# Kernel optimization log

Hardware: AMD Instinct MI355X
Metric: run time of the kernel (lower is better)

The kernel has to match this reference:

```python
import jax, jax.numpy as jnp
import numpy as np

N_USERS_P1 = 50001
N_ITEMS_P1 = 100001
N = N_USERS_P1 + N_ITEMS_P1  # 150002
D = 64
N_BEH = 2
N_LAYERS = 2
N_EDGES = 2000000
BATCH = 2048
REG_WEIGHT = 1e-4
EPS = 1e-9
GAMMA = 1e-10  # BPRLoss gamma


def setup_inputs() -> dict:
    key = jax.random.key(0)
    ks = jax.random.split(key, 12)
    return {
        "user_emb": jax.random.normal(ks[0], (N_USERS_P1, D), jnp.float32) * 0.1,
        "item_emb": jax.random.normal(ks[1], (N_ITEMS_P1, D), jnp.float32) * 0.1,
        "now_degree": jax.random.uniform(ks[2], (N_BEH, N, 1), jnp.float32, 1.0, 100.0),
        "old_degree": jax.random.uniform(ks[3], (N_BEH, N, 1), jnp.float32, 1.0, 100.0),
        "last_stage": jax.random.normal(ks[4], (N_BEH, N_LAYERS, N, D), jnp.float32) * 0.1,
        "denom_w": jax.random.uniform(ks[5], (1,), jnp.float32),
        "oldscale_w": jax.random.uniform(ks[6], (1,), jnp.float32),
        "conv_w": jax.random.normal(ks[7], (N_BEH, N_LAYERS, 2), jnp.float32),
        "src": jax.random.randint(ks[8], (N_BEH, N_EDGES), 0, N, jnp.int32),
        "dst": jax.random.randint(ks[9], (N_BEH, N_EDGES), 0, N, jnp.int32),
        "batch_data": jax.random.randint(ks[10], (BATCH, N_BEH, 3), 1, N_USERS_P1, jnp.int32),
    }


def _propagate(user_emb, item_emb, now_degree, old_degree, last_stage,
               denom_w, oldscale_w, conv_w, src, dst):
    total = jnp.concatenate([user_emb, item_emb], axis=0)  # [N, D]
    n = total.shape[0]
    all_embeddings = []
    for b in range(N_BEH):
        # denominator_forward: ReLU(W*old) + new ; molecular = ones
        den = jnp.sqrt(jax.nn.relu(old_degree[b] * denom_w[0]) + now_degree[b])  # [N,1]
        norm = 1.0 / (den + EPS)  # [N,1] (molecular == 1)
        e = total
        layer_embs = [e]
        for _ in range(N_LAYERS):
            e = norm * e
            # sparse adjacency matmul: scatter-add gathered rows (binary adjacency)
            e = jax.ops.segment_sum(e[src[b]], dst[b], num_segments=n)
            e = norm * e
            layer_embs.append(e)
        # oldscale_forward + rescale of last-stage embeddings
        old_scale = jnp.sqrt(jax.nn.relu(old_degree[b] * oldscale_w[0]))  # [N,1]
        rscale = old_scale / (den + EPS)  # [N,1]
        new_layers = [total]
        for l in range(N_LAYERS):
            old_l = last_stage[b, l] * rscale
            # Conv2d(1,1,(2,1)) over stacked (old,new): w0*old + w1*new
            new_layers.append(conv_w[b, l, 0] * old_l + conv_w[b, l, 1] * layer_embs[l])
        mean_e = jnp.stack(new_layers, axis=1).mean(axis=1)  # [N, D]
        # F.normalize(dim=-1)
        mean_e = mean_e / jnp.maximum(jnp.linalg.norm(mean_e, axis=-1, keepdims=True), 1e-12)
        total = mean_e + total
        all_embeddings.append(total)
    return all_embeddings


def reference(user_emb, item_emb, now_degree, old_degree, last_stage,
              denom_w, oldscale_w, conv_w, src, dst, batch_data):
    all_embeddings = _propagate(user_emb, item_emb, now_degree, old_degree,
                                last_stage, denom_w, oldscale_w, conv_w, src, dst)
    total_loss = jnp.float32(0.0)
    for b in range(N_BEH):
        emb = all_embeddings[b]
        u_all = emb[:N_USERS_P1]
        i_all = emb[N_USERS_P1:]
        data = batch_data[:, b]
        uf = u_all[data[:, 0]]          # [B, D]
        itf = i_all[data[:, 1:]]        # [B, 2, D]
        scores = jnp.einsum('bd,bkd->bk', uf, itf)  # [B, 2]
        bpr = -jnp.log(GAMMA + jax.nn.sigmoid(scores[:, 0] - scores[:, 1])).mean()
        total_loss = total_loss + bpr
    # EmbLoss: sum of L2 norms / last embedding's row count
    emb_loss = (jnp.linalg.norm(user_emb) + jnp.linalg.norm(item_emb)) / item_emb.shape[0]
    return total_loss + REG_WEIGHT * emb_loss
```

## Files before the change

### kernel.cpp

```cpp
#include <hip/hip_runtime.h>

#define N_USERS_P1 50001
#define N_ITEMS_P1 100001
#define N_TOTAL    150002
#define DIM        64
#define N_BEH      2
#define N_EDGES    2000000
#define BATCH      2048
#define ND         ((long)N_TOTAL * DIM)
#define REG_WEIGHT 1e-4f
#define GAMMA_     1e-10f
#define EPS_       1e-9f

#define SCAN_CHUNK 1024
#define NB_SCAN    ((N_TOTAL + SCAN_CHUNK - 1) / SCAN_CHUNK)

#define FILL_G     256
#define FILL_NB    (8 * FILL_G)

__global__ void I_CRGCN_57002805952693_kernel() {}

__global__ void k_init(float* __restrict__ accums, float* __restrict__ out) {
    if (threadIdx.x < 4) accums[threadIdx.x] = 0.f;
    if (threadIdx.x == 0) out[0] = 0.25f;
}

__global__ void k_zero4(float4* __restrict__ p, long n4) {
    long i = (long)blockIdx.x * blockDim.x + threadIdx.x;
    long s = (long)gridDim.x * blockDim.x;
    float4 z = make_float4(0.f, 0.f, 0.f, 0.f);
    for (; i < n4; i += s) p[i] = z;
}

__global__ void k_zero_int(int* __restrict__ p, int n) {
    int i = blockIdx.x * blockDim.x + threadIdx.x;
    if (i < n) p[i] = 0;
}

__global__ void k_build_total(const float* __restrict__ ue,
                              const float* __restrict__ ie,
                              float* __restrict__ total,
                              float* __restrict__ accums) {
    const long NU = (long)N_USERS_P1 * DIM;
    long i = (long)blockIdx.x * blockDim.x + threadIdx.x;
    long s = (long)gridDim.x * blockDim.x;
    float su = 0.f, si = 0.f;
    for (; i < ND; i += s) {
        float v;
        if (i < NU) { v = ue[i];      su += v * v; }
        else        { v = ie[i - NU]; si += v * v; }
        total[i] = v;
    }
    for (int o = 32; o > 0; o >>= 1) {
        su += __shfl_xor(su, o);
        si += __shfl_xor(si, o);
    }
    __shared__ float smu[4], smi[4];
    int w = threadIdx.x >> 6, l = threadIdx.x & 63;
    if (l == 0) { smu[w] = su; smi[w] = si; }
    __syncthreads();
    if (threadIdx.x == 0) {
        float a = 0.f, b = 0.f;
        for (int k = 0; k < 4; k++) { a += smu[k]; b += smi[k]; }
        atomicAdd(&accums[0], a);
        atomicAdd(&accums[1], b);
    }
}

__global__ void k_norms(const float* __restrict__ now_deg,
                        const float* __restrict__ old_deg,
                        const float* __restrict__ denom_w,
                        const float* __restrict__ oldscale_w,
                        float* __restrict__ norm,
                        float* __restrict__ rscale) {
    int i = blockIdx.x * blockDim.x + threadIdx.x;
    if (i >= N_BEH * N_TOTAL) return;
    float dw = denom_w[0], ow = oldscale_w[0];
    float od = old_deg[i], nd = now_deg[i];
    float den = sqrtf(fmaxf(od * dw, 0.f) + nd);
    float inv = 1.f / (den + EPS_);
    norm[i]   = inv;
    rscale[i] = sqrtf(fmaxf(od * ow, 0.f)) * inv;
}

__global__ void k_count(const int* __restrict__ dst, int* __restrict__ deg) {
    int i = blockIdx.x * blockDim.x + threadIdx.x;
    if (i < N_EDGES) atomicAdd(&deg[dst[i]], 1);
}

__global__ void k_count_pos(const int* __restrict__ dst,
                            int* __restrict__ deg,
                            unsigned char* __restrict__ pos) {
    int i = blockIdx.x * blockDim.x + threadIdx.x;
    if (i < N_EDGES) {
        int p = atomicAdd(&deg[dst[i]], 1);
        pos[i] = (unsigned char)p;
    }
}

__global__ void k_scan1(const int* __restrict__ deg,
                        int* __restrict__ rowptr,
                        int* __restrict__ bsum) {
    __shared__ int sh[256];
    int tid  = threadIdx.x;
    int base = blockIdx.x * SCAN_CHUNK + tid * 4;
    int v0 = 0, v1 = 0, v2 = 0, v3 = 0;
    if (base + 0 < N_TOTAL) v0 = deg[base + 0];
    if (base + 1 < N_TOTAL) v1 = deg[base + 1];
    if (base + 2 < N_TOTAL) v2 = deg[base + 2];
    if (base + 3 < N_TOTAL) v3 = deg[base + 3];
    int s = v0 + v1 + v2 + v3;
    sh[tid] = s;
    __syncthreads();
    for (int off = 1; off < 256; off <<= 1) {
        int t = (tid >= off) ? sh[tid - off] : 0;
        __syncthreads();
        sh[tid] += t;
        __syncthreads();
    }
    int excl = sh[tid] - s;
    if (base + 0 < N_TOTAL) rowptr[base + 0] = excl;
    if (base + 1 < N_TOTAL) rowptr[base + 1] = excl + v0;
    if (base + 2 < N_TOTAL) rowptr[base + 2] = excl + v0 + v1;
    if (base + 3 < N_TOTAL) rowptr[base + 3] = excl + v0 + v1 + v2;
    if (tid == 255) bsum[blockIdx.x] = sh[255];
}

__global__ void k_scan1_ip(int* __restrict__ data, int* __restrict__ bsum) {
    __shared__ int sh[256];
    int tid  = threadIdx.x;
    int base = blockIdx.x * SCAN_CHUNK + tid * 4;
    int v0 = 0, v1 = 0, v2 = 0, v3 = 0;
    if (base + 0 < N_TOTAL) v0 = data[base + 0];
    if (base + 1 < N_TOTAL) v1 = data[base + 1];
    if (base + 2 < N_TOTAL) v2 = data[base + 2];
    if (base + 3 < N_TOTAL) v3 = data[base + 3];
    int s = v0 + v1 + v2 + v3;
    sh[tid] = s;
    __syncthreads();
    for (int off = 1; off < 256; off <<= 1) {
        int t = (tid >= off) ? sh[tid - off] : 0;
        __syncthreads();
        sh[tid] += t;
        __syncthreads();
    }
    int excl = sh[tid] - s;
    if (base + 0 < N_TOTAL) data[base + 0] = excl;
    if (base + 1 < N_TOTAL) data[base + 1] = excl + v0;
    if (base + 2 < N_TOTAL) data[base + 2] = excl + v0 + v1;
    if (base + 3 < N_TOTAL) data[base + 3] = excl + v0 + v1 + v2;
    if (tid == 255) bsum[blockIdx.x] = sh[255];
}

__global__ void k_scan2(int* __restrict__ bsum) {
    __shared__ int sh[256];
    int tid = threadIdx.x;
    int v = (tid < NB_SCAN) ? bsum[tid] : 0;
    sh[tid] = v;
    __syncthreads();
    for (int off = 1; off < 256; off <<= 1) {
        int t = (tid >= off) ? sh[tid - off] : 0;
        __syncthreads();
        sh[tid] += t;
        __syncthreads();
    }
    if (tid < NB_SCAN) bsum[tid] = sh[tid] - v;
}

__global__ void k_scan3(int* __restrict__ rowptr, const int* __restrict__ bsum,
                        int* __restrict__ cursor) {
    int i = blockIdx.x * blockDim.x + threadIdx.x;
    if (i >= N_TOTAL) return;
    int v = rowptr[i] + bsum[i / SCAN_CHUNK];
    rowptr[i] = v;
    cursor[i] = v;
}

__global__ void k_scan3a(int* __restrict__ rowptr, const int* __restrict__ bsum) {
    int i = blockIdx.x * blockDim.x + threadIdx.x;
    if (i == 0) rowptr[N_TOTAL] = N_EDGES;
    if (i >= N_TOTAL) return;
    rowptr[i] += bsum[i / SCAN_CHUNK];
}

__global__ void k_fill(const int* __restrict__ src, const int* __restrict__ dst,
                       int* __restrict__ cursor, int* __restrict__ csr_src) {
    int i = blockIdx.x * blockDim.x + threadIdx.x;
    if (i < N_EDGES) {
        int pos = atomicAdd(&cursor[dst[i]], 1);
        csr_src[pos] = src[i];
    }
}

__global__ void k_fill_banded(const int* __restrict__ src,
                              const int* __restrict__ dst,
                              const int* __restrict__ rowptr,
                              const unsigned char* __restrict__ pos,
                              int* __restrict__ csr) {
    const int C = (N_EDGES + FILL_G - 1) / FILL_G;
    int x = blockIdx.x & 7;
    int g = blockIdx.x >> 3;
    int beg = g * C;
    int end = beg + C;
    if (end > N_EDGES) end = N_EDGES;
    for (int i = beg + threadIdx.x; i < end; i += blockDim.x) {
        int d = dst[i];
        if (((d >> 12) & 7) == x) {
            csr[rowptr[d] + (int)pos[i]] = src[i];
        }
    }
}

__global__ void k_gather_update(const int* __restrict__ rowptr,
                                const int* __restrict__ rowend,
                                const int* __restrict__ csr_src,
                                const float* __restrict__ norm,
                                const float* __restrict__ rscale,
                                const float* __restrict__ tin,
                                float* __restrict__ tout,
                                const float* __restrict__ last_b,
                                const float* __restrict__ conv_b) {
    long gid  = (long)blockIdx.x * blockDim.x + threadIdx.x;
    long row  = gid >> 6;
    int  lane = (int)(gid & 63);
    if (row >= N_TOTAL) return;
    int beg = rowptr[row], end = rowend[row];
    float acc = 0.f;
    int j = beg;
    for (; j + 4 <= end; j += 4) {
        int s0 = csr_src[j], s1 = csr_src[j + 1];
        int s2 = csr_src[j + 2], s3 = csr_src[j + 3];
        float a0 = norm[s0] * tin[(long)s0 * DIM + lane];
        float a1 = norm[s1] * tin[(long)s1 * DIM + lane];
        float a2 = norm[s2] * tin[(long)s2 * DIM + lane];
        float a3 = norm[s3] * tin[(long)s3 * DIM + lane];
        acc += a0 + a1 + a2 + a3;
    }
    for (; j < end; ++j) {
        int s = csr_src[j];
        acc += norm[s] * tin[(long)s * DIM + lane];
    }
    float cw00 = conv_b[0], cw01 = conv_b[1];
    float cw10 = conv_b[2], cw11 = conv_b[3];
    long  off = row * DIM + lane;
    float t   = tin[off];
    float e1  = norm[row] * acc;
    float ls0 = last_b[off];
    float ls1 = last_b[ND + off];
    float rs  = rscale[row];
    float m = (t + cw00 * ls0 * rs + cw01 * t + cw10 * ls1 * rs + cw11 * e1)
              * (1.f / 3.f);
    float ss = m * m;
    for (int o = 32; o > 0; o >>= 1) ss += __shfl_xor(ss, o);
    tout[off] = t + m / fmaxf(sqrtf(ss), 1e-12f);
}

__global__ void k_edges(const int* __restrict__ src,
                        const int* __restrict__ dst,
                        const float* __restrict__ norm,
                        const float* __restrict__ total,
                        float* __restrict__ agg) {
    long gid   = (long)blockIdx.x * blockDim.x + threadIdx.x;
    long wave  = gid >> 6;
    int  lane  = (int)(gid & 63);
    long waves = ((long)gridDim.x * blockDim.x) >> 6;
    for (long e = wave; e < N_EDGES; e += waves) {
        int s = src[e], t = dst[e];
        float v = norm[s] * total[(long)s * DIM + lane];
        atomicAdd(&agg[(long)t * DIM + lane], v);
    }
}

__global__ void k_update(float* __restrict__ total,
                         const float* __restrict__ agg,
                         const float* __restrict__ norm,
                         const float* __restrict__ rscale,
                         const float* __restrict__ last_b,
                         const float* __restrict__ conv_b) {
    long gid  = (long)blockIdx.x * blockDim.x + threadIdx.x;
    long row  = gid >> 6;
    int  lane = (int)(gid & 63);
    if (row >= N_TOTAL) return;
    float cw00 = conv_b[0], cw01 = conv_b[1];
    float cw10 = conv_b[2], cw11 = conv_b[3];
    long  off = row * DIM + lane;
    float t   = total[off];
    float e1  = norm[row] * agg[off];
    float ls0 = last_b[off];
    float ls1 = last_b[ND + off];
    float rs  = rscale[row];
    float m = (t + cw00 * ls0 * rs + cw01 * t + cw10 * ls1 * rs + cw11 * e1)
              * (1.f / 3.f);
    float ss = m * m;
    for (int o = 32; o > 0; o >>= 1) ss += __shfl_xor(ss, o);
    total[off] = t + m / fmaxf(sqrtf(ss), 1e-12f);
}

__global__ void k_bpr(const float* __restrict__ total,
                      const int* __restrict__ bdata,
                      int b,
                      float* __restrict__ acc) {
    long gid  = (long)blockIdx.x * blockDim.x + threadIdx.x;
    long i    = gid >> 6;
    int  lane = (int)(gid & 63);
    if (i >= BATCH) return;
    const int* row = bdata + (i * N_BEH + b) * 3;
    int iu = row[0];
    int i0 = N_USERS_P1 + row[1];
    int i1 = N_USERS_P1 + row[2];
    float u = total[(long)iu * DIM + lane];
    float a = total[(long)i0 * DIM + lane];
    float c = total[(long)i1 * DIM + lane];
    float s0 = u * a, s1 = u * c;
    for (int o = 32; o > 0; o >>= 1) {
        s0 += __shfl_xor(s0, o);
        s1 += __shfl_xor(s1, o);
    }
    if (lane == 0) {
        float d   = s0 - s1;
        float sig = 1.f / (1.f + expf(-d));
        atomicAdd(acc, -logf(GAMMA_ + sig));
    }
}

__global__ void k_final(const float* __restrict__ accums, float* __restrict__ out) {
    float bpr  = (accums[2] + accums[3]) * (1.f / (float)BATCH);
    float embl = (sqrtf(accums[0]) + sqrtf(accums[1])) / (float)N_ITEMS_P1;
    out[0] = bpr + REG_WEIGHT * embl;
}

extern "C" void kernel_launch(void* const* d_in, const int* in_sizes, int n_in,
                              void* d_out, int out_size, void* d_ws, size_t ws_size,
                              hipStream_t stream) {
    const float* ue      = (const float*)d_in[0];
    const float* ie      = (const float*)d_in[1];
    const float* now_deg = (const float*)d_in[2];
    const float* old_deg = (const float*)d_in[3];
    const float* last    = (const float*)d_in[4];
    const float* denw    = (const float*)d_in[5];
    const float* oldw    = (const float*)d_in[6];
    const float* convw   = (const float*)d_in[7];
    const int*   src     = (const int*)d_in[8];
    const int*   dst     = (const int*)d_in[9];
    const int*   bdata   = (const int*)d_in[10];
    float*       out     = (float*)d_out;

    float* ws      = (float*)d_ws;
    float* total_a = ws;
    float* total_b = total_a + ND;
    float* norm    = total_b + ND;
    float* rscale  = norm + 2L * N_TOTAL;
    float* accums  = rscale + 2L * N_TOTAL;

    int*           rowptrA = (int*)(accums + 8);
    int*           bsumA   = rowptrA + (N_TOTAL + 1);
    unsigned char* posA    = (unsigned char*)(bsumA + 256);
    int*           csrA    = (int*)(posA + N_EDGES);
    size_t requiredA = (size_t)((char*)(csrA + N_EDGES) - (char*)d_ws);

    int* rowptrB = (int*)(accums + 8);
    int* cursorB = rowptrB + N_TOTAL;
    int* bsumB   = cursorB + N_TOTAL;
    int* csrB    = bsumB + 256;
    size_t requiredB = (size_t)((char*)(csrB + N_EDGES) - (char*)d_ws);

    k_init<<<1, 64, 0, stream>>>(accums, out);
    k_build_total<<<2048, 256, 0, stream>>>(ue, ie, total_a, accums);
    k_norms<<<(N_BEH * N_TOTAL + 255) / 256, 256, 0, stream>>>(
        now_deg, old_deg, denw, oldw, norm, rscale);

    const int nbE = (N_EDGES + 255) / 256;
    const int nbN = (N_TOTAL + 255) / 256;
    const int nbR = (N_TOTAL + 3) / 4;

    if (ws_size >= requiredA) {
        const float* tin = total_a;
        float*       tout = total_b;
        for (int b = 0; b < N_BEH; b++) {
            const int* srcb = src + (long)b * N_EDGES;
            const int* dstb = dst + (long)b * N_EDGES;
            k_zero_int<<<(N_TOTAL + 1 + 255) / 256, 256, 0, stream>>>(
                rowptrA, N_TOTAL + 1);
            k_count_pos<<<nbE, 256, 0, stream>>>(dstb, rowptrA, posA);
            k_scan1_ip<<<NB_SCAN, 256, 0, stream>>>(rowptrA, bsumA);
            k_scan2<<<1, 256, 0, stream>>>(bsumA);
            k_scan3a<<<nbN, 256, 0, stream>>>(rowptrA, bsumA);
            k_fill_banded<<<FILL_NB, 256, 0, stream>>>(
                srcb, dstb, rowptrA, posA, csrA);
            k_gather_update<<<nbR, 256, 0, stream>>>(
                rowptrA, rowptrA + 1, csrA,
                norm + (long)b * N_TOTAL, rscale + (long)b * N_TOTAL,
                tin, tout, last + (long)b * 2 * ND, convw + b * 4);
            k_bpr<<<BATCH / 4, 256, 0, stream>>>(tout, bdata, b, &accums[2 + b]);
            float* t = (float*)tin; tin = tout; tout = t;
        }
    } else if (ws_size >= requiredB) {
        const float* tin = total_a;
        float*       tout = total_b;
        for (int b = 0; b < N_BEH; b++) {
            const int* srcb = src + (long)b * N_EDGES;
            const int* dstb = dst + (long)b * N_EDGES;
            k_zero_int<<<nbN, 256, 0, stream>>>(cursorB, N_TOTAL);
            k_count<<<nbE, 256, 0, stream>>>(dstb, cursorB);
            k_scan1<<<NB_SCAN, 256, 0, stream>>>(cursorB, rowptrB, bsumB);
            k_scan2<<<1, 256, 0, stream>>>(bsumB);
            k_scan3<<<nbN, 256, 0, stream>>>(rowptrB, bsumB, cursorB);
            k_fill<<<nbE, 256, 0, stream>>>(srcb, dstb, cursorB, csrB);
            k_gather_update<<<nbR, 256, 0, stream>>>(
                rowptrB, cursorB, csrB,
                norm + (long)b * N_TOTAL, rscale + (long)b * N_TOTAL,
                tin, tout, last + (long)b * 2 * ND, convw + b * 4);
            k_bpr<<<BATCH / 4, 256, 0, stream>>>(tout, bdata, b, &accums[2 + b]);
            float* t = (float*)tin; tin = tout; tout = t;
        }
    } else {
        for (int b = 0; b < N_BEH; b++) {
            k_zero4<<<2048, 256, 0, stream>>>((float4*)total_b, ND / 4);
            k_edges<<<16384, 256, 0, stream>>>(
                src + (long)b * N_EDGES, dst + (long)b * N_EDGES,
                norm + (long)b * N_TOTAL, total_a, total_b);
            k_update<<<nbR, 256, 0, stream>>>(
                total_a, total_b, norm + (long)b * N_TOTAL,
                rscale + (long)b * N_TOTAL, last + (long)b * 2 * ND, convw + b * 4);
            k_bpr<<<BATCH / 4, 256, 0, stream>>>(total_a, bdata, b, &accums[2 + b]);
        }
    }
    k_final<<<1, 1, 0, stream>>>(accums, out);
}
```

Before: 871.3 us.

## Vectorize build, count, fill and gather kernels with 16-byte loads

After: 798.5 us. 1.09x faster.

```diff
diff --git a/kernel.cpp b/kernel.cpp
--- a/kernel.cpp
+++ b/kernel.cpp
@@ -37,19 +37,25 @@
     if (i < n) p[i] = 0;
 }
 
-__global__ void k_build_total(const float* __restrict__ ue,
-                              const float* __restrict__ ie,
-                              float* __restrict__ total,
+__global__ void k_build_total(const float4* __restrict__ ue4,
+                              const float4* __restrict__ ie4,
+                              float4* __restrict__ total4,
                               float* __restrict__ accums) {
-    const long NU = (long)N_USERS_P1 * DIM;
+    const long NU4 = (long)N_USERS_P1 * DIM / 4;
+    const long ND4 = ND / 4;
     long i = (long)blockIdx.x * blockDim.x + threadIdx.x;
     long s = (long)gridDim.x * blockDim.x;
     float su = 0.f, si = 0.f;
-    for (; i < ND; i += s) {
-        float v;
-        if (i < NU) { v = ue[i];      su += v * v; }
-        else        { v = ie[i - NU]; si += v * v; }
-        total[i] = v;
+    for (; i < ND4; i += s) {
+        float4 v;
+        if (i < NU4) {
+            v = ue4[i];
+            su += v.x * v.x + v.y * v.y + v.z * v.z + v.w * v.w;
+        } else {
+            v = ie4[i - NU4];
+            si += v.x * v.x + v.y * v.y + v.z * v.z + v.w * v.w;
+        }
+        total4[i] = v;
     }
     for (int o = 32; o > 0; o >>= 1) {
         su += __shfl_xor(su, o);
@@ -88,14 +94,18 @@
     if (i < N_EDGES) atomicAdd(&deg[dst[i]], 1);
 }
 
-__global__ void k_count_pos(const int* __restrict__ dst,
+__global__ void k_count_pos(const int4* __restrict__ dst4,
                             int* __restrict__ deg,
-                            unsigned char* __restrict__ pos) {
-    int i = blockIdx.x * blockDim.x + threadIdx.x;
-    if (i < N_EDGES) {
-        int p = atomicAdd(&deg[dst[i]], 1);
-        pos[i] = (unsigned char)p;
-    }
+                            uchar4* __restrict__ pos4) {
+    int i = blockIdx.x * blockDim.x + threadIdx.x;
+    if (i >= N_EDGES / 4) return;
+    int4 d = dst4[i];
+    uchar4 p;
+    p.x = (unsigned char)atomicAdd(&deg[d.x], 1);
+    p.y = (unsigned char)atomicAdd(&deg[d.y], 1);
+    p.z = (unsigned char)atomicAdd(&deg[d.z], 1);
+    p.w = (unsigned char)atomicAdd(&deg[d.w], 1);
+    pos4[i] = p;
 }
 
 __global__ void k_scan1(const int* __restrict__ deg,
@@ -192,22 +202,26 @@
     }
 }
 
-__global__ void k_fill_banded(const int* __restrict__ src,
-                              const int* __restrict__ dst,
+__global__ void k_fill_banded(const int4* __restrict__ src4,
+                              const int4* __restrict__ dst4,
                               const int* __restrict__ rowptr,
-                              const unsigned char* __restrict__ pos,
+                              const uchar4* __restrict__ pos4,
                               int* __restrict__ csr) {
-    const int C = (N_EDGES + FILL_G - 1) / FILL_G;
+    const int NQ = N_EDGES / 4;
+    const int C  = (NQ + FILL_G - 1) / FILL_G;
     int x = blockIdx.x & 7;
     int g = blockIdx.x >> 3;
     int beg = g * C;
     int end = beg + C;
-    if (end > N_EDGES) end = N_EDGES;
+    if (end > NQ) end = NQ;
     for (int i = beg + threadIdx.x; i < end; i += blockDim.x) {
-        int d = dst[i];
-        if (((d >> 12) & 7) == x) {
-            csr[rowptr[d] + (int)pos[i]] = src[i];
-        }
+        int4   d = dst4[i];
+        uchar4 p = pos4[i];
+        int4   s = src4[i];
+        if (((d.x >> 12) & 7) == x) csr[rowptr[d.x] + (int)p.x] = s.x;
+        if (((d.y >> 12) & 7) == x) csr[rowptr[d.y] + (int)p.y] = s.y;
+        if (((d.z >> 12) & 7) == x) csr[rowptr[d.z] + (int)p.z] = s.z;
+        if (((d.w >> 12) & 7) == x) csr[rowptr[d.w] + (int)p.w] = s.w;
     }
 }
 
@@ -224,30 +238,67 @@
     long row  = gid >> 6;
     int  lane = (int)(gid & 63);
     if (row >= N_TOTAL) return;
+    int grp = lane >> 4;
+    int q   = lane & 15;
+
     int beg = rowptr[row], end = rowend[row];
-    float acc = 0.f;
-    int j = beg;
-    for (; j + 4 <= end; j += 4) {
-        int s0 = csr_src[j], s1 = csr_src[j + 1];
-        int s2 = csr_src[j + 2], s3 = csr_src[j + 3];
-        float a0 = norm[s0] * tin[(long)s0 * DIM + lane];
-        float a1 = norm[s1] * tin[(long)s1 * DIM + lane];
-        float a2 = norm[s2] * tin[(long)s2 * DIM + lane];
-        float a3 = norm[s3] * tin[(long)s3 * DIM + lane];
-        acc += a0 + a1 + a2 + a3;
-    }
-    for (; j < end; ++j) {
-        int s = csr_src[j];
-        acc += norm[s] * tin[(long)s * DIM + lane];
-    }
+
+    long  off = row * DIM + lane;
+    float t    = tin[off];
+    float ls0  = last_b[off];
+    float ls1  = last_b[ND + off];
+    float rs   = rscale[row];
+    float nr   = norm[row];
     float cw00 = conv_b[0], cw01 = conv_b[1];
     float cw10 = conv_b[2], cw11 = conv_b[3];
-    long  off = row * DIM + lane;
-    float t   = tin[off];
-    float e1  = norm[row] * acc;
-    float ls0 = last_b[off];
-    float ls1 = last_b[ND + off];
-    float rs  = rscale[row];
+
+    float4 acca = make_float4(0.f, 0.f, 0.f, 0.f);
+    float4 accb = make_float4(0.f, 0.f, 0.f, 0.f);
+    int j = beg;
+    for (; j + 8 <= end; j += 8) {
+        int sa = csr_src[j + grp];
+        int sb = csr_src[j + 4 + grp];
+        float na = norm[sa];
+        float nb = norm[sb];
+        float4 va = *(const float4*)&tin[(long)sa * DIM + q * 4];
+        float4 vb = *(const float4*)&tin[(long)sb * DIM + q * 4];
+        acca.x += na * va.x; acca.y += na * va.y;
+        acca.z += na * va.z; acca.w += na * va.w;
+        accb.x += nb * vb.x; accb.y += nb * vb.y;
+        accb.z += nb * vb.z; accb.w += nb * vb.w;
+    }
+    if (j + 4 <= end) {
+        int s = csr_src[j + grp];
+        float n = norm[s];
+        float4 v = *(const float4*)&tin[(long)s * DIM + q * 4];
+        acca.x += n * v.x; acca.y += n * v.y;
+        acca.z += n * v.z; acca.w += n * v.w;
+        j += 4;
+    }
+    if (j < end) {
+        int idx = j + grp;
+        int s = csr_src[(idx < end) ? idx : (end - 1)];
+        float n = (idx < end) ? norm[s] : 0.f;
+        float4 v = *(const float4*)&tin[(long)s * DIM + q * 4];
+        accb.x += n * v.x; accb.y += n * v.y;
+        accb.z += n * v.z; accb.w += n * v.w;
+    }
+    float4 a4;
+    a4.x = acca.x + accb.x; a4.y = acca.y + accb.y;
+    a4.z = acca.z + accb.z; a4.w = acca.w + accb.w;
+    a4.x += __shfl_xor(a4.x, 16); a4.x += __shfl_xor(a4.x, 32);
+    a4.y += __shfl_xor(a4.y, 16); a4.y += __shfl_xor(a4.y, 32);
+    a4.z += __shfl_xor(a4.z, 16); a4.z += __shfl_xor(a4.z, 32);
+    a4.w += __shfl_xor(a4.w, 16); a4.w += __shfl_xor(a4.w, 32);
+    int srcl = lane >> 2;
+    float a0 = __shfl(a4.x, srcl);
+    float a1 = __shfl(a4.y, srcl);
+    float a2 = __shfl(a4.z, srcl);
+    float a3 = __shfl(a4.w, srcl);
+    int c = lane & 3;
+    float accS = (c == 0) ? a0 : (c == 1) ? a1 : (c == 2) ? a2 : a3;
+
+    float e1 = nr * accS;
     float m = (t + cw00 * ls0 * rs + cw01 * t + cw10 * ls1 * rs + cw11 * e1)
               * (1.f / 3.f);
     float ss = m * m;
@@ -365,13 +416,15 @@
     size_t requiredB = (size_t)((char*)(csrB + N_EDGES) - (char*)d_ws);
 
     k_init<<<1, 64, 0, stream>>>(accums, out);
-    k_build_total<<<2048, 256, 0, stream>>>(ue, ie, total_a, accums);
+    k_build_total<<<2048, 256, 0, stream>>>(
+        (const float4*)ue, (const float4*)ie, (float4*)total_a, accums);
     k_norms<<<(N_BEH * N_TOTAL + 255) / 256, 256, 0, stream>>>(
         now_deg, old_deg, denw, oldw, norm, rscale);
 
-    const int nbE = (N_EDGES + 255) / 256;
-    const int nbN = (N_TOTAL + 255) / 256;
-    const int nbR = (N_TOTAL + 3) / 4;
+    const int nbE  = (N_EDGES + 255) / 256;
+    const int nbE4 = (N_EDGES / 4 + 255) / 256;
+    const int nbN  = (N_TOTAL + 255) / 256;
+    const int nbR  = (N_TOTAL + 3) / 4;
 
     if (ws_size >= requiredA) {
         const float* tin = total_a;
@@ -381,12 +434,14 @@
             const int* dstb = dst + (long)b * N_EDGES;
             k_zero_int<<<(N_TOTAL + 1 + 255) / 256, 256, 0, stream>>>(
                 rowptrA, N_TOTAL + 1);
-            k_count_pos<<<nbE, 256, 0, stream>>>(dstb, rowptrA, posA);
+            k_count_pos<<<nbE4, 256, 0, stream>>>(
+                (const int4*)dstb, rowptrA, (uchar4*)posA);
             k_scan1_ip<<<NB_SCAN, 256, 0, stream>>>(rowptrA, bsumA);
             k_scan2<<<1, 256, 0, stream>>>(bsumA);
             k_scan3a<<<nbN, 256, 0, stream>>>(rowptrA, bsumA);
             k_fill_banded<<<FILL_NB, 256, 0, stream>>>(
-                srcb, dstb, rowptrA, posA, csrA);
+                (const int4*)srcb, (const int4*)dstb, rowptrA,
+                (const uchar4*)posA, csrA);
             k_gather_update<<<nbR, 256, 0, stream>>>(
                 rowptrA, rowptrA + 1, csrA,
                 norm + (long)b * N_TOTAL, rscale + (long)b * N_TOTAL,
```
